# Kernel tuning notes

Measured on AMD Instinct MI355X. Metric: run time of the kernel, lower is better.

Reference implementation:

```python
import jax, jax.numpy as jnp
import numpy as np

B, S = 4, 1024          # 4 prefill sequences of length 1024 (cu_seqlens equal-length)
D_MODEL = 2048
N_HEADS = 32
N_KV_HEADS = 8
HEAD_DIM = D_MODEL // N_HEADS          # 64
GROUPS = N_HEADS // N_KV_HEADS         # 4
ROPE_THETA = 10000.0
SCALE = HEAD_DIM ** -0.5


def setup_inputs() -> dict:
    key = jax.random.key(0)
    ks = jax.random.split(key, 6)
    T = B * S
    hidden_states = jax.random.normal(ks[0], (T, D_MODEL), jnp.float32)
    # rotary tables: positions restart per sequence (prefill)
    pos = jnp.tile(jnp.arange(S, dtype=jnp.float32), B)            # [T]
    inv_freq = 1.0 / (ROPE_THETA ** (jnp.arange(0, HEAD_DIM, 2, dtype=jnp.float32) / HEAD_DIM))
    freqs = pos[:, None] * inv_freq[None, :]                        # [T, HEAD_DIM/2]
    cos, sin = jnp.cos(freqs), jnp.sin(freqs)
    std = D_MODEL ** -0.5
    Wq = jax.random.normal(ks[1], (D_MODEL, N_HEADS * HEAD_DIM), jnp.float32) * std
    Wk = jax.random.normal(ks[2], (D_MODEL, N_KV_HEADS * HEAD_DIM), jnp.float32) * std
    Wv = jax.random.normal(ks[3], (D_MODEL, N_KV_HEADS * HEAD_DIM), jnp.float32) * std
    Wo = jax.random.normal(ks[4], (N_HEADS * HEAD_DIM, D_MODEL), jnp.float32) * std
    return {"hidden_states": hidden_states, "cos": cos, "sin": sin,
            "Wq": Wq, "Wk": Wk, "Wv": Wv, "Wo": Wo}


def _rope(x, cos, sin):
    # NeoX-style rotary: x [T, H, D], cos/sin [T, D/2]
    half = x.shape[-1] // 2
    x1, x2 = x[..., :half], x[..., half:]
    c, s = cos[:, None, :], sin[:, None, :]
    return jnp.concatenate([x1 * c - x2 * s, x2 * c + x1 * s], axis=-1)


def reference(hidden_states, cos, sin, Wq, Wk, Wv, Wo):
    T = hidden_states.shape[0]
    q = (hidden_states @ Wq).reshape(T, N_HEADS, HEAD_DIM)
    k = (hidden_states @ Wk).reshape(T, N_KV_HEADS, HEAD_DIM)
    v = (hidden_states @ Wv).reshape(T, N_KV_HEADS, HEAD_DIM)
    q = _rope(q, cos, sin)
    k = _rope(k, cos, sin)
    # equal-length varlen prefill -> [B, S, H, D]
    q = q.reshape(B, S, N_HEADS, HEAD_DIM)
    k = jnp.repeat(k.reshape(B, S, N_KV_HEADS, HEAD_DIM), GROUPS, axis=2)  # GQA expand
    v = jnp.repeat(v.reshape(B, S, N_KV_HEADS, HEAD_DIM), GROUPS, axis=2)
    scores = jnp.einsum("bqhd,bkhd->bhqk", q, k) * SCALE
    causal = jnp.tril(jnp.ones((S, S), dtype=bool))
    scores = jnp.where(causal[None, None], scores, jnp.finfo(scores.dtype).min)
    probs = jax.nn.softmax(scores, axis=-1)
    attn = jnp.einsum("bhqk,bkhd->bqhd", probs, v).reshape(T, N_HEADS * HEAD_DIM)
    return attn @ Wo
```

## Files before the change

kernel.cpp:

```cpp
#include <hip/hip_runtime.h>
#include <type_traits>


typedef __bf16 bf16x8 __attribute__((ext_vector_type(8)));
typedef __bf16 bf16x4 __attribute__((ext_vector_type(4)));
typedef float f32x4 __attribute__((ext_vector_type(4)));
typedef unsigned short u16;
typedef unsigned int u32;

#define DEVI __device__ __forceinline__

DEVI u16 f2bf(float f) {
  u32 u = __builtin_bit_cast(u32, f);
  u += 0x7FFF + ((u >> 16) & 1);
  return (u16)(u >> 16);
}

DEVI void ld16_lds(const void* g, void* l) {
  __builtin_amdgcn_global_load_lds((const __attribute__((address_space(1))) u32*)g,
                                   (__attribute__((address_space(3))) u32*)l, 16, 0, 0);
}

__global__ __launch_bounds__(256) void convert_f32_bf16(const float* __restrict__ src,
                                                        u16* __restrict__ dst, int n4) {
  int i = blockIdx.x * 256 + threadIdx.x;
  if (i >= n4) return;
  float4 v = ((const float4*)src)[i];
  ushort4 o;
  o.x = f2bf(v.x); o.y = f2bf(v.y); o.z = f2bf(v.z); o.w = f2bf(v.w);
  ((ushort4*)dst)[i] = o;
}

__global__ __launch_bounds__(256) void trans_f32_bf16(const float* __restrict__ src,
                                                      u16* __restrict__ dst, int R, int C,
                                                      float scale) {
  __shared__ float tile[32][33];
  int c0 = blockIdx.x * 32, r0 = blockIdx.y * 32;
  int tx = threadIdx.x & 31, ty = threadIdx.x >> 5;
#pragma unroll
  for (int i = 0; i < 32; i += 8)
    tile[ty + i][tx] = src[(size_t)(r0 + ty + i) * C + (c0 + tx)];
  __syncthreads();
#pragma unroll
  for (int i = 0; i < 32; i += 8)
    dst[(size_t)(c0 + ty + i) * R + (r0 + tx)] = f2bf(tile[tx][ty + i] * scale);
}

template <typename OutT, bool ROPE, int BN, int GM, int GN, int WM, int WN>
__global__ __launch_bounds__(512, 2) void gemm_bt(const u16* __restrict__ A,
                                                  const u16* __restrict__ BT,
                                                  OutT* __restrict__ C, int M, int N, int K,
                                                  const float* __restrict__ cs,
                                                  const float* __restrict__ sn) {
  static_assert(GM * GN == 8 && 16 * WM * GM == 256 && 16 * WN * GN == BN, "geom");
  __shared__ u16 As[2][256 * 64];
  __shared__ u16 Bs[2][BN * 64];
  const int tid = threadIdx.x;
  const int lane = tid & 63, wave = tid >> 6;
  const int quad = lane >> 4, l16 = lane & 15;
  const int m0 = blockIdx.y * 256, n0 = blockIdx.x * BN;
  const int wr = wave / GN, wc = wave % GN;

  f32x4 acc[WM][WN] = {};

  auto stageTile = [&](int t, int bufIdx) {
    const int k0 = t * 64;
    u16* Ad = &As[bufIdx][0];
    u16* Bd = &Bs[bufIdx][0];
#pragma unroll
    for (int i = 0; i < 4; ++i) {
      int id = i * 512 + tid;
      int row = id >> 3, ch = id & 7;
      int sch = ch ^ (row & 7);
      ld16_lds(A + (size_t)(m0 + row) * K + k0 + sch * 8, Ad + id * 8);
    }
#pragma unroll
    for (int i = 0; i < BN / 64; ++i) {
      int id = i * 512 + tid;
      int row = id >> 3, ch = id & 7;
      int sch = ch ^ (row & 7);
      ld16_lds(BT + (size_t)(n0 + row) * K + k0 + sch * 8, Bd + id * 8);
    }
  };

  const int NT = K / 64;
  stageTile(0, 0);
  __syncthreads();

  for (int t = 0; t < NT; ++t) {
    const int c = t & 1;
    if (t + 1 < NT) stageTile(t + 1, 1 - c);
    const u16* Ab = &As[c][0];
    const u16* Bb = &Bs[c][0];
#pragma unroll
    for (int ks = 0; ks < 2; ++ks) {
      bf16x8 bfv[WN];
#pragma unroll
      for (int j = 0; j < WN; ++j) {
        int rb = wc * (16 * WN) + j * 16 + l16;
        bfv[j] = *(const bf16x8*)&Bb[rb * 64 + (((ks * 4 + quad) ^ (rb & 7)) * 8)];
      }
#pragma unroll
      for (int mh = 0; mh < WM / 4; ++mh) {
        bf16x8 af[4];
#pragma unroll
        for (int i = 0; i < 4; ++i) {
          int r = wr * (16 * WM) + (mh * 4 + i) * 16 + l16;
          af[i] = *(const bf16x8*)&Ab[r * 64 + (((ks * 4 + quad) ^ (r & 7)) * 8)];
        }
        __builtin_amdgcn_s_setprio(1);
#pragma unroll
        for (int i = 0; i < 4; ++i)
#pragma unroll
          for (int j = 0; j < WN; ++j)
            acc[mh * 4 + i][j] =
                __builtin_amdgcn_mfma_f32_16x16x32_bf16(af[i], bfv[j], acc[mh * 4 + i][j], 0, 0, 0);
        __builtin_amdgcn_s_setprio(0);
      }
    }
    __syncthreads();
  }

  if constexpr (ROPE) {
    if (n0 + wc * (16 * WN) < 2560) {
#pragma unroll
      for (int i = 0; i < WM; i++) {
        int t0 = m0 + wr * (16 * WM) + i * 16 + quad * 4;
#pragma unroll
        for (int jj = 0; jj < 2; jj++) {
          int d = jj * 16 + l16;
#pragma unroll
          for (int r = 0; r < 4; r++) {
            float cv = cs[(size_t)(t0 + r) * 32 + d];
            float sv = sn[(size_t)(t0 + r) * 32 + d];
            float x1 = acc[i][jj][r], x2 = acc[i][jj + 2][r];
            acc[i][jj][r] = x1 * cv - x2 * sv;
            acc[i][jj + 2][r] = x2 * cv + x1 * sv;
          }
        }
      }
    }
  }

#pragma unroll
  for (int i = 0; i < WM; i++) {
    int row = m0 + wr * (16 * WM) + i * 16 + quad * 4;
#pragma unroll
    for (int j = 0; j < WN; j++) {
      int col = n0 + wc * (16 * WN) + j * 16 + l16;
#pragma unroll
      for (int r = 0; r < 4; r++) {
        size_t off = (size_t)(row + r) * N + col;
        if constexpr (sizeof(OutT) == 2) C[off] = f2bf(acc[i][j][r]);
        else C[off] = acc[i][j][r];
      }
    }
  }
}

__global__ __launch_bounds__(256) void vkt_build(const u16* __restrict__ qkv,
                                                 u16* __restrict__ vkt) {
  __shared__ u16 Vn[128 * 64];
  const int kt = blockIdx.x, kvh = blockIdx.y, b = blockIdx.z;
  const int tid = threadIdx.x;
  const u16* src = qkv + ((size_t)b * 1024 + kt * 128) * 3072 + 2560 + kvh * 64;
  {
    int tok = tid >> 1, hf = tid & 1;
    const uint4* s4 = (const uint4*)(src + (size_t)tok * 3072 + hf * 32);
    uint4* d4 = (uint4*)&Vn[tok * 64 + hf * 32];
#pragma unroll
    for (int j = 0; j < 4; j++) d4[j] = s4[j];
  }
  __syncthreads();
  u16* img = vkt + ((((size_t)b * 8 + kvh) * 8 + kt) << 13);
#pragma unroll
  for (int i = 0; i < 4; i++) {
    int c = tid * 4 + i;
    int dd = c >> 4, chsw = c & 15;
    int ch = chsw ^ (dd & 15);
    u16 tmp[8];
#pragma unroll
    for (int p = 0; p < 8; p++) {
      int col = ch * 8 + p;
      int g = col >> 5, kl = col & 31;
      int kph = ((kl >> 2) & 1) * 16 + ((kl >> 4) & 1) * 8 + ((kl >> 3) & 1) * 4 + (kl & 3);
      tmp[p] = Vn[(g * 32 + kph) * 64 + dd];
    }
    *(uint4*)&img[c * 8] = *(const uint4*)tmp;
  }
}

__global__ __launch_bounds__(256, 2) void flash_attn(const u16* __restrict__ qkv,
                                                     const u16* __restrict__ vkt,
                                                     u16* __restrict__ attn) {
  __shared__ u16 Ks[2][128 * 64];
  __shared__ u16 VT[2][64 * 128];

  const int tid = threadIdx.x;
  const int lane = tid & 63, wave = tid >> 6;
  const int quad = lane >> 4, l16 = lane & 15;
  const int qtA = blockIdx.x, qtB = 7 - blockIdx.x;
  const int h = blockIdx.y, b = blockIdx.z, kvh = h >> 2;
  const size_t tokBase = (size_t)b * 1024;
  const int qcol = h * 64, kcol = 2048 + kvh * 64;
  const int srow = tid >> 3, spc = tid & 7, ssc = spc ^ (srow & 7);

  auto stageK = [&](const u16* gbase, u16* L) {
#pragma unroll
    for (int i = 0; i < 4; i++)
      ld16_lds(gbase + (size_t)(srow + i * 32) * 3072 + ssc * 8, &L[tid * 8 + i * 2048]);
  };
  const u16* vimg = vkt + (((size_t)b * 8 + kvh) << 16);
  auto stageV = [&](int kt, u16* L) {
    const u16* g = vimg + ((size_t)kt << 13);
#pragma unroll
    for (int i = 0; i < 4; i++)
      ld16_lds(g + i * 2048 + tid * 8, &L[tid * 8 + i * 2048]);
  };

  stageK(qkv + (tokBase + qtA * 128) * 3072 + qcol, Ks[0]);
  stageK(qkv + (tokBase + qtB * 128) * 3072 + qcol, Ks[1]);
  __syncthreads();
  bf16x8 qfA[2][2], qfB[2][2];
#pragma unroll
  for (int nq = 0; nq < 2; nq++) {
    int qrow = wave * 32 + nq * 16 + l16;
#pragma unroll
    for (int ks = 0; ks < 2; ks++) {
      int c = (ks * 4 + quad) ^ (qrow & 7);
      qfA[nq][ks] = *(const bf16x8*)&Ks[0][qrow * 64 + c * 8];
      qfB[nq][ks] = *(const bf16x8*)&Ks[1][qrow * 64 + c * 8];
    }
  }
  __syncthreads();

  float lA[2] = {0.f, 0.f}, lB[2] = {0.f, 0.f};
  f32x4 oA[4][2] = {}, oB[4][2] = {};

  auto proc = [&](const bf16x8 (&kf)[2][2], const bf16x8 (&va)[4], const bf16x8 (&qf)[2][2],
                  f32x4 (&o)[4][2], float (&lacc)[2], bool msk, int c) {
    f32x4 s[2][2] = {};
#pragma unroll
    for (int mkl = 0; mkl < 2; mkl++)
#pragma unroll
      for (int ks = 0; ks < 2; ks++) {
        s[0][mkl] = __builtin_amdgcn_mfma_f32_16x16x32_bf16(kf[mkl][ks], qf[0][ks], s[0][mkl], 0, 0, 0);
        s[1][mkl] = __builtin_amdgcn_mfma_f32_16x16x32_bf16(kf[mkl][ks], qf[1][ks], s[1][mkl], 0, 0, 0);
      }
    if (msk) {
#pragma unroll
      for (int nq = 0; nq < 2; nq++) {
        int q = wave * 32 + nq * 16 + l16;
#pragma unroll
        for (int mkl = 0; mkl < 2; mkl++)
#pragma unroll
          for (int r = 0; r < 4; r++)
            if ((c * 2 + mkl) * 16 + quad * 4 + r > q) s[nq][mkl][r] = -3e38f;
      }
    }
    bf16x8 pf[2];
#pragma unroll
    for (int nq = 0; nq < 2; nq++) {
      float a0 = 0.f;
#pragma unroll
      for (int mkl = 0; mkl < 2; mkl++)
#pragma unroll
        for (int r = 0; r < 4; r++) {
          float p = __builtin_amdgcn_exp2f(s[nq][mkl][r]);
          s[nq][mkl][r] = p;
          a0 += p;
        }
      lacc[nq] += a0;
      pf[nq][0] = (__bf16)s[nq][0][0]; pf[nq][1] = (__bf16)s[nq][0][1];
      pf[nq][2] = (__bf16)s[nq][0][2]; pf[nq][3] = (__bf16)s[nq][0][3];
      pf[nq][4] = (__bf16)s[nq][1][0]; pf[nq][5] = (__bf16)s[nq][1][1];
      pf[nq][6] = (__bf16)s[nq][1][2]; pf[nq][7] = (__bf16)s[nq][1][3];
    }
#pragma unroll
    for (int md = 0; md < 4; md++) {
      o[md][0] = __builtin_amdgcn_mfma_f32_16x16x32_bf16(va[md], pf[0], o[md][0], 0, 0, 0);
      o[md][1] = __builtin_amdgcn_mfma_f32_16x16x32_bf16(va[md], pf[1], o[md][1], 0, 0, 0);
    }
  };

  stageK(qkv + tokBase * 3072 + kcol, Ks[0]);
  stageV(0, VT[0]);

  for (int kt = 0; kt <= qtB; kt++) {
    const int cur = kt & 1;
    __syncthreads();
    if (kt < qtB) {
      stageK(qkv + (tokBase + (kt + 1) * 128) * 3072 + kcol, Ks[1 - cur]);
      stageV(kt + 1, VT[1 - cur]);
    }
    const bool doA = (kt <= qtA), mA = (kt == qtA), mB = (kt == qtB);
    const u16* K = Ks[cur];
    const u16* V = VT[cur];
#pragma unroll
    for (int c = 0; c < 4; c++) {
      bf16x8 kf[2][2];
#pragma unroll
      for (int mkl = 0; mkl < 2; mkl++) {
        int krow = (c * 2 + mkl) * 16 + l16;
#pragma unroll
        for (int ks = 0; ks < 2; ks++)
          kf[mkl][ks] = *(const bf16x8*)&K[krow * 64 + ((ks * 4 + quad) ^ (krow & 7)) * 8];
      }
      bf16x8 va[4];
#pragma unroll
      for (int md = 0; md < 4; md++) {
        int dd = md * 16 + l16;
        va[md] = *(const bf16x8*)&V[dd * 128 + ((c * 4 + quad) ^ l16) * 8];
      }
      proc(kf, va, qfB, oB, lB, mB, c);
      if (doA) proc(kf, va, qfA, oA, lA, mA, c);
    }
  }

  auto epilogue = [&](const f32x4 (&o)[4][2], const float (&lacc)[2], int qt_tile) {
#pragma unroll
    for (int nq = 0; nq < 2; nq++) {
      float l = lacc[nq];
      l += __shfl_xor(l, 16);
      l += __shfl_xor(l, 32);
      float inv = 1.0f / l;
      int t = qt_tile * 128 + wave * 32 + nq * 16 + l16;
      size_t rowOff = (tokBase + t) * 2048 + qcol;
#pragma unroll
      for (int md = 0; md < 4; md++) {
        bf16x4 w;
        w[0] = (__bf16)(o[md][nq][0] * inv);
        w[1] = (__bf16)(o[md][nq][1] * inv);
        w[2] = (__bf16)(o[md][nq][2] * inv);
        w[3] = (__bf16)(o[md][nq][3] * inv);
        *(bf16x4*)&attn[rowOff + md * 16 + quad * 4] = w;
      }
    }
  };
  epilogue(oB, lB, qtB);
  epilogue(oA, lA, qtA);
}

extern "C" void kernel_launch(void* const* d_in, const int* in_sizes, int n_in,
                              void* d_out, int out_size, void* d_ws, size_t ws_size,
                              hipStream_t stream) {
  const float* hs = (const float*)d_in[0];
  const float* cs = (const float*)d_in[1];
  const float* sn = (const float*)d_in[2];
  const float* Wq = (const float*)d_in[3];
  const float* Wk = (const float*)d_in[4];
  const float* Wv = (const float*)d_in[5];
  const float* Wo = (const float*)d_in[6];
  float* out = (float*)d_out;

  char* ws = (char*)d_ws;
  u16* hsB   = (u16*)(ws);
  u16* vkt   = (u16*)(ws);
  u16* wqkvT = (u16*)(ws + 16777216);
  u16* woT   = (u16*)(ws + 29360128);
  u16* qkv   = (u16*)(ws + 37748736);
  u16* attnB = (u16*)(ws + 62914560);

  const float QSCALE = 0.18033688011112042f;

  convert_f32_bf16<<<8192, 256, 0, stream>>>(hs, hsB, 4096 * 2048 / 4);
  trans_f32_bf16<<<dim3(64, 64), 256, 0, stream>>>(Wq, wqkvT, 2048, 2048, QSCALE);
  trans_f32_bf16<<<dim3(16, 64), 256, 0, stream>>>(Wk, wqkvT + (size_t)2048 * 2048, 2048, 512, 1.0f);
  trans_f32_bf16<<<dim3(16, 64), 256, 0, stream>>>(Wv, wqkvT + (size_t)2560 * 2048, 2048, 512, 1.0f);
  trans_f32_bf16<<<dim3(64, 64), 256, 0, stream>>>(Wo, woT, 2048, 2048, 1.0f);

  gemm_bt<u16, true, 256, 2, 4, 8, 4><<<dim3(12, 16), 512, 0, stream>>>(
      hsB, wqkvT, qkv, 4096, 3072, 2048, cs, sn);
  vkt_build<<<dim3(8, 8, 4), 256, 0, stream>>>(qkv, vkt);
  flash_attn<<<dim3(4, 32, 4), 256, 0, stream>>>(qkv, vkt, attnB);
  gemm_bt<float, false, 128, 4, 2, 4, 4><<<dim3(16, 16), 512, 0, stream>>>(
      attnB, woT, out, 4096, 2048, 2048, nullptr, nullptr);
}
```

Before: 281.8 us.

## Rewrite GEMM main loop as 8-phase ping-pong schedule with split half-tile staging

Replaces the double-buffered GEMM loop with a hand-scheduled loop that processes two K-tiles per iteration in eight phases. Each phase interleaves LDS fragment loads, half-tile global-to-LDS prefetches and a quarter of the MFMA work, using explicit vmcnt/lgkmcnt waits and barriers instead of one full __syncthreads per tile. The wave grid is fixed at 2x4 with 128 rows per wave for both GEMMs, which changes the output projection's wave tiling. The aim is to overlap memory traffic with MFMA issue more finely, at the cost of many more barriers and fragile, hand-tuned wait counts.

Result: no change. 276.8 us (-1.8%).

```diff
diff --git a/kernel.cpp b/kernel.cpp
--- a/kernel.cpp
+++ b/kernel.cpp
@@ -20,6 +20,18 @@
   __builtin_amdgcn_global_load_lds((const __attribute__((address_space(1))) u32*)g,
                                    (__attribute__((address_space(3))) u32*)l, 16, 0, 0);
 }
+
+template <int N> DEVI void waitvm() {
+  if constexpr (N == 0) asm volatile("s_waitcnt vmcnt(0)" ::: "memory");
+  else if constexpr (N == 3) asm volatile("s_waitcnt vmcnt(3)" ::: "memory");
+  else if constexpr (N == 4) asm volatile("s_waitcnt vmcnt(4)" ::: "memory");
+  else static_assert(N == 0, "unsupported vmcnt");
+}
+DEVI void lgkm0() {
+  asm volatile("s_waitcnt lgkmcnt(0)" ::: "memory");
+  __builtin_amdgcn_sched_barrier(0);
+}
+DEVI void barrier() { __builtin_amdgcn_s_barrier(); }
 
 __global__ __launch_bounds__(256) void convert_f32_bf16(const float* __restrict__ src,
                                                         u16* __restrict__ dst, int n4) {
@@ -46,86 +58,149 @@
     dst[(size_t)(c0 + ty + i) * R + (r0 + tx)] = f2bf(tile[tx][ty + i] * scale);
 }
 
-template <typename OutT, bool ROPE, int BN, int GM, int GN, int WM, int WN>
-__global__ __launch_bounds__(512, 2) void gemm_bt(const u16* __restrict__ A,
-                                                  const u16* __restrict__ BT,
-                                                  OutT* __restrict__ C, int M, int N, int K,
-                                                  const float* __restrict__ cs,
-                                                  const float* __restrict__ sn) {
-  static_assert(GM * GN == 8 && 16 * WM * GM == 256 && 16 * WN * GN == BN, "geom");
+template <typename OutT, bool ROPE, int BN>
+__global__ __launch_bounds__(512, 2) void gemm8(const u16* __restrict__ A,
+                                                const u16* __restrict__ BT,
+                                                OutT* __restrict__ C, int M, int N, int K,
+                                                const float* __restrict__ cs,
+                                                const float* __restrict__ sn) {
+  constexpr int WN = BN / 64;
+  constexpr int NH = WN / 2;
+  constexpr int LB = BN / 128;
+  constexpr int VMP = 2 + LB;
   __shared__ u16 As[2][256 * 64];
   __shared__ u16 Bs[2][BN * 64];
   const int tid = threadIdx.x;
   const int lane = tid & 63, wave = tid >> 6;
   const int quad = lane >> 4, l16 = lane & 15;
   const int m0 = blockIdx.y * 256, n0 = blockIdx.x * BN;
-  const int wr = wave / GN, wc = wave % GN;
-
-  f32x4 acc[WM][WN] = {};
-
-  auto stageTile = [&](int t, int bufIdx) {
-    const int k0 = t * 64;
-    u16* Ad = &As[bufIdx][0];
-    u16* Bd = &Bs[bufIdx][0];
-#pragma unroll
-    for (int i = 0; i < 4; ++i) {
+  const int wr = wave >> 2, wc = wave & 3;
+
+  f32x4 acc[8][WN] = {};
+
+  auto stageA = [&](int t, int h) {
+    u16* D = &As[t & 1][h * 8192];
+    const u16* G = A + (size_t)m0 * K + t * 64;
+#pragma unroll
+    for (int i = 0; i < 2; ++i) {
       int id = i * 512 + tid;
-      int row = id >> 3, ch = id & 7;
-      int sch = ch ^ (row & 7);
-      ld16_lds(A + (size_t)(m0 + row) * K + k0 + sch * 8, Ad + id * 8);
-    }
-#pragma unroll
-    for (int i = 0; i < BN / 64; ++i) {
+      int row = h * 128 + (id >> 3), ch = id & 7;
+      ld16_lds(G + (size_t)row * K + (ch ^ (row & 7)) * 8, D + id * 8);
+    }
+  };
+  auto stageB = [&](int t, int h) {
+    u16* D = &Bs[t & 1][h * (BN / 2) * 64];
+    const u16* G = BT + (size_t)n0 * K + t * 64;
+#pragma unroll
+    for (int i = 0; i < LB; ++i) {
       int id = i * 512 + tid;
-      int row = id >> 3, ch = id & 7;
-      int sch = ch ^ (row & 7);
-      ld16_lds(BT + (size_t)(n0 + row) * K + k0 + sch * 8, Bd + id * 8);
-    }
+      int row = h * (BN / 2) + (id >> 3), ch = id & 7;
+      ld16_lds(G + (size_t)row * K + (ch ^ (row & 7)) * 8, D + id * 8);
+    }
+  };
+
+  bf16x8 af[4][2], bv0[NH][2], bv1[NH][2];
+  auto ldA = [&](int msub, int d) {
+#pragma unroll
+    for (int i = 0; i < 4; ++i)
+#pragma unroll
+      for (int ks = 0; ks < 2; ++ks) {
+        int r = wr * 128 + msub * 64 + i * 16 + l16;
+        af[i][ks] = *(const bf16x8*)&As[d][r * 64 + (((ks * 4 + quad) ^ (r & 7)) * 8)];
+      }
+  };
+  auto ldB = [&](bf16x8 (&bv)[NH][2], int nsub, int d) {
+#pragma unroll
+    for (int j = 0; j < NH; ++j)
+#pragma unroll
+      for (int ks = 0; ks < 2; ++ks) {
+        int rb = wc * (16 * WN) + (nsub * NH + j) * 16 + l16;
+        bv[j][ks] = *(const bf16x8*)&Bs[d][rb * 64 + (((ks * 4 + quad) ^ (rb & 7)) * 8)];
+      }
+  };
+  auto mm = [&](const bf16x8 (&bv)[NH][2], int mo, int no) {
+    __builtin_amdgcn_s_setprio(1);
+#pragma unroll
+    for (int i = 0; i < 4; ++i)
+#pragma unroll
+      for (int j = 0; j < NH; ++j)
+#pragma unroll
+        for (int ks = 0; ks < 2; ++ks)
+          acc[mo + i][no + j] =
+              __builtin_amdgcn_mfma_f32_16x16x32_bf16(af[i][ks], bv[j][ks], acc[mo + i][no + j], 0, 0, 0);
+    __builtin_amdgcn_s_setprio(0);
   };
 
   const int NT = K / 64;
-  stageTile(0, 0);
-  __syncthreads();
-
-  for (int t = 0; t < NT; ++t) {
-    const int c = t & 1;
-    if (t + 1 < NT) stageTile(t + 1, 1 - c);
-    const u16* Ab = &As[c][0];
-    const u16* Bb = &Bs[c][0];
-#pragma unroll
-    for (int ks = 0; ks < 2; ++ks) {
-      bf16x8 bfv[WN];
-#pragma unroll
-      for (int j = 0; j < WN; ++j) {
-        int rb = wc * (16 * WN) + j * 16 + l16;
-        bfv[j] = *(const bf16x8*)&Bb[rb * 64 + (((ks * 4 + quad) ^ (rb & 7)) * 8)];
-      }
-#pragma unroll
-      for (int mh = 0; mh < WM / 4; ++mh) {
-        bf16x8 af[4];
-#pragma unroll
-        for (int i = 0; i < 4; ++i) {
-          int r = wr * (16 * WM) + (mh * 4 + i) * 16 + l16;
-          af[i] = *(const bf16x8*)&Ab[r * 64 + (((ks * 4 + quad) ^ (r & 7)) * 8)];
-        }
-        __builtin_amdgcn_s_setprio(1);
-#pragma unroll
-        for (int i = 0; i < 4; ++i)
-#pragma unroll
-          for (int j = 0; j < WN; ++j)
-            acc[mh * 4 + i][j] =
-                __builtin_amdgcn_mfma_f32_16x16x32_bf16(af[i], bfv[j], acc[mh * 4 + i][j], 0, 0, 0);
-        __builtin_amdgcn_s_setprio(0);
-      }
-    }
-    __syncthreads();
+
+  stageA(0, 0); stageA(0, 1); stageB(0, 0); stageB(0, 1);
+  stageB(1, 0); stageA(1, 0);
+  waitvm<VMP>();
+  barrier();
+
+#pragma unroll 1
+  for (int T = 0; T < NT; T += 2) {
+    const bool pf = (T + 2 < NT);
+    ldA(0, 0); ldB(bv0, 0, 0);
+    stageA(T + 1, 1);
+    barrier(); lgkm0();
+    mm(bv0, 0, 0);
+    barrier();
+
+    ldB(bv1, 1, 0);
+    stageB(T + 1, 1);
+    barrier(); lgkm0();
+    mm(bv1, 0, NH);
+    barrier();
+
+    ldA(1, 0);
+    if (pf) stageB(T + 2, 0);
+    barrier(); lgkm0();
+    mm(bv1, 4, NH);
+    barrier();
+
+    if (pf) { stageA(T + 2, 0); waitvm<VMP>(); }
+    else waitvm<0>();
+    barrier();
+    __builtin_amdgcn_sched_barrier(0);
+    mm(bv0, 4, 0);
+    barrier();
+
+    ldA(0, 1); ldB(bv0, 0, 1);
+    if (pf) stageB(T + 2, 1);
+    barrier(); lgkm0();
+    mm(bv0, 0, 0);
+    barrier();
+
+    ldB(bv1, 1, 1);
+    if (pf) stageA(T + 2, 1);
+    barrier(); lgkm0();
+    mm(bv1, 0, NH);
+    barrier();
+
+    ldA(1, 1);
+    if (pf) stageB(T + 3, 0);
+    barrier(); lgkm0();
+    mm(bv1, 4, NH);
+    barrier();
+
+    if (pf) {
+      stageA(T + 3, 0);
+      waitvm<VMP>();
+      barrier();
+      __builtin_amdgcn_sched_barrier(0);
+      mm(bv0, 4, 0);
+      barrier();
+    } else {
+      mm(bv0, 4, 0);
+    }
   }
 
   if constexpr (ROPE) {
     if (n0 + wc * (16 * WN) < 2560) {
 #pragma unroll
-      for (int i = 0; i < WM; i++) {
-        int t0 = m0 + wr * (16 * WM) + i * 16 + quad * 4;
+      for (int i = 0; i < 8; i++) {
+        int t0 = m0 + wr * 128 + i * 16 + quad * 4;
 #pragma unroll
         for (int jj = 0; jj < 2; jj++) {
           int d = jj * 16 + l16;
@@ -143,8 +218,8 @@
   }
 
 #pragma unroll
-  for (int i = 0; i < WM; i++) {
-    int row = m0 + wr * (16 * WM) + i * 16 + quad * 4;
+  for (int i = 0; i < 8; i++) {
+    int row = m0 + wr * 128 + i * 16 + quad * 4;
 #pragma unroll
     for (int j = 0; j < WN; j++) {
       int col = n0 + wc * (16 * WN) + j * 16 + l16;
@@ -369,10 +444,10 @@
   trans_f32_bf16<<<dim3(16, 64), 256, 0, stream>>>(Wv, wqkvT + (size_t)2560 * 2048, 2048, 512, 1.0f);
   trans_f32_bf16<<<dim3(64, 64), 256, 0, stream>>>(Wo, woT, 2048, 2048, 1.0f);
 
-  gemm_bt<u16, true, 256, 2, 4, 8, 4><<<dim3(12, 16), 512, 0, stream>>>(
+  gemm8<u16, true, 256><<<dim3(12, 16), 512, 0, stream>>>(
       hsB, wqkvT, qkv, 4096, 3072, 2048, cs, sn);
   vkt_build<<<dim3(8, 8, 4), 256, 0, stream>>>(qkv, vkt);
   flash_attn<<<dim3(4, 32, 4), 256, 0, stream>>>(qkv, vkt, attnB);
-  gemm_bt<float, false, 128, 4, 2, 4, 4><<<dim3(16, 16), 512, 0, stream>>>(
+  gemm8<float, false, 128><<<dim3(16, 16), 512, 0, stream>>>(
       attnB, woT, out, 4096, 2048, 2048, nullptr, nullptr);
 }
```
